# Kernel tuning notes

Measured on AMD Instinct MI355X. Metric: run time of the kernel, lower is better.

## Reference

```python
import jax, jax.numpy as jnp
import numpy as np

B, H, W, C, WS, NH, NL, ND = 64, 32, 32, 96, 8, 6, 4, 6
N = WS * WS
HD = C // NH
SC = HD ** -0.5


def _rel_pos_index():
    coords = np.stack(np.meshgrid(np.arange(WS), np.arange(WS), indexing='ij')).reshape(2, -1)
    rel = (coords[:, :, None] - coords[:, None, :]).transpose(1, 2, 0)
    rel[..., 0] += WS - 1
    rel[..., 1] += WS - 1
    rel[..., 0] *= 2 * WS - 1
    return jnp.asarray(rel.sum(-1))  # [N, N] int


def _attn_mask():
    shift = WS // 2
    img = np.zeros((H, W))
    cnt = 0
    for hs in (slice(0, -WS), slice(-WS, -shift), slice(-shift, None)):
        for ws_ in (slice(0, -WS), slice(-WS, -shift), slice(-shift, None)):
            img[hs, ws_] = cnt
            cnt += 1
    mw = img.reshape(H // WS, WS, W // WS, WS).transpose(0, 2, 1, 3).reshape(-1, N)
    am = mw[:, None, :] - mw[:, :, None]
    return jnp.asarray(np.where(am != 0, -100.0, 0.0).astype(np.float32))  # [nW, N, N]


RPI = _rel_pos_index()
AMASK = _attn_mask()


def ln(x, s, b):
    m = x.mean(-1, keepdims=True)
    v = ((x - m) ** 2).mean(-1, keepdims=True)
    return (x - m) * jax.lax.rsqrt(v + 1e-5) * s + b


def conv3(x, w, b):
    return jax.lax.conv_general_dilated(x, w, (1, 1), 'SAME', dimension_numbers=('NHWC', 'HWIO', 'NHWC')) + b


def win_part(x):  # (B,H,W,C) -> (B*nW, N, C)
    b = x.shape[0]
    return x.reshape(b, H // WS, WS, W // WS, WS, C).transpose(0, 1, 3, 2, 4, 5).reshape(-1, N, C)


def win_rev(xw, b):  # (B*nW, N, C) -> (B,H,W,C)
    return xw.reshape(b, H // WS, W // WS, WS, WS, C).transpose(0, 1, 3, 2, 4, 5).reshape(b, H, W, C)


def swin_block(x, shift, p):
    n1s, n1b, qw, qb, pw, pb, rpb, n2s, n2b, f1w, f1b, f2w, f2b = p
    b = x.shape[0]
    h = ln(x, n1s, n1b).reshape(b, H, W, C)
    if shift:
        h = jnp.roll(h, (-shift, -shift), (1, 2))
    xw = win_part(h)
    qkv = (xw @ qw + qb).reshape(-1, N, 3, NH, HD).transpose(2, 0, 3, 1, 4)
    q, k, v = qkv[0], qkv[1], qkv[2]  # each (B*nW, NH, N, HD)
    attn = (q * SC) @ k.transpose(0, 1, 3, 2)  # (B*nW, NH, N, N)
    bias = rpb[RPI.reshape(-1)].reshape(N, N, NH).transpose(2, 0, 1)
    attn = attn + bias[None]
    if shift:
        nW = AMASK.shape[0]
        attn = (attn.reshape(b, nW, NH, N, N) + AMASK[None, :, None]).reshape(-1, NH, N, N)
    attn = jax.nn.softmax(attn, -1)
    o = (attn @ v).transpose(0, 2, 1, 3).reshape(-1, N, C) @ pw + pb
    h = win_rev(o, b)
    if shift:
        h = jnp.roll(h, (shift, shift), (1, 2))
    x = x + h.reshape(b, H * W, C)
    y = ln(x, n2s, n2b)
    return x + jax.nn.gelu(y @ f1w + f1b, approximate=False) @ f2w + f2b


def setup_inputs() -> dict:
    key = jax.random.key(0)
    ks = iter(jax.random.split(key, 40))
    nrm = lambda shape: jax.random.normal(next(ks), shape, jnp.float32) * 0.02
    d = {
        'es_input': jax.random.normal(next(ks), (B, 2, H, W), jnp.float32),
        'j_plus_input': jax.random.normal(next(ks), (B, 2, H, W), jnp.float32),
        'conv_first_w': nrm((3, 3, 4, C)), 'conv_first_b': jnp.zeros((C,), jnp.float32),
        'pe_norm_s': jnp.ones((C,), jnp.float32), 'pe_norm_b': jnp.zeros((C,), jnp.float32),
        'n1_s': jnp.ones((NL, ND, C), jnp.float32), 'n1_b': jnp.zeros((NL, ND, C), jnp.float32),
        'qkv_w': nrm((NL, ND, C, 3 * C)), 'qkv_b': jnp.zeros((NL, ND, 3 * C), jnp.float32),
        'proj_w': nrm((NL, ND, C, C)), 'proj_b': jnp.zeros((NL, ND, C), jnp.float32),
        'rpb': nrm((NL, ND, (2 * WS - 1) ** 2, NH)),
        'n2_s': jnp.ones((NL, ND, C), jnp.float32), 'n2_b': jnp.zeros((NL, ND, C), jnp.float32),
        'fc1_w': nrm((NL, ND, C, 4 * C)), 'fc1_b': jnp.zeros((NL, ND, 4 * C), jnp.float32),
        'fc2_w': nrm((NL, ND, 4 * C, C)), 'fc2_b': jnp.zeros((NL, ND, C), jnp.float32),
        'rstb_conv_w': nrm((NL, 3, 3, C, C)), 'rstb_conv_b': jnp.zeros((NL, C), jnp.float32),
        'normf_s': jnp.ones((C,), jnp.float32), 'normf_b': jnp.zeros((C,), jnp.float32),
        'body_w': nrm((3, 3, C, C)), 'body_b': jnp.zeros((C,), jnp.float32),
        'last_w': nrm((3, 3, C, 2)), 'last_b': jnp.zeros((2,), jnp.float32),
    }
    return d


def reference(es_input, j_plus_input, conv_first_w, conv_first_b, pe_norm_s, pe_norm_b,
              n1_s, n1_b, qkv_w, qkv_b, proj_w, proj_b, rpb, n2_s, n2_b,
              fc1_w, fc1_b, fc2_w, fc2_b, rstb_conv_w, rstb_conv_b,
              normf_s, normf_b, body_w, body_b, last_w, last_b):
    x0 = jnp.concatenate([es_input, j_plus_input], 1).transpose(0, 2, 3, 1)  # NHWC, C=4
    xf = conv3(x0, conv_first_w, conv_first_b)  # shallow feature, [B,H,W,96]
    x = ln(xf.reshape(B, H * W, C), pe_norm_s, pe_norm_b)  # patch_embed norm
    for l in range(NL):
        r = x
        for d in range(ND):
            p = (n1_s[l, d], n1_b[l, d], qkv_w[l, d], qkv_b[l, d], proj_w[l, d], proj_b[l, d],
                 rpb[l, d], n2_s[l, d], n2_b[l, d], fc1_w[l, d], fc1_b[l, d], fc2_w[l, d], fc2_b[l, d])
            x = swin_block(x, 0 if d % 2 == 0 else WS // 2, p)
        x = conv3(x.reshape(B, H, W, C), rstb_conv_w[l], rstb_conv_b[l]).reshape(B, H * W, C) + r
    x = ln(x, normf_s, normf_b).reshape(B, H, W, C)
    res = conv3(x, body_w, body_b) + xf
    out = conv3(res, last_w, last_b)  # [B,H,W,2]
    return out.transpose(0, 3, 1, 2)
```

## Files before the change

kernel.cpp:

```cpp
#include <hip/hip_runtime.h>
#include <hip/hip_bf16.h>
#include <cstddef>
#include <cstdint>

#define BB 64
#define HH 32
#define WW_ 32
#define CC 96
#define WS 8
#define NH 6
#define NL 4
#define ND 6
#define T_TOK (BB*HH*WW_)
#define TC ((size_t)T_TOK*CC)

typedef long long ll;
typedef __attribute__((ext_vector_type(8))) short short8;
typedef __attribute__((ext_vector_type(4))) float f32x4;
typedef __attribute__((ext_vector_type(4))) unsigned short ushort4v;

__global__ void JNetSwinIR_41034117546277_kernel() {}

__device__ __forceinline__ unsigned short f2bf(float f) {
  unsigned u = __float_as_uint(f);
  unsigned r = (u + 0x7FFF + ((u >> 16) & 1)) >> 16;
  return (unsigned short)r;
}
__device__ __forceinline__ float bf2f(unsigned short h) {
  return __uint_as_float(((unsigned)h) << 16);
}

__global__ __launch_bounds__(256) void fill_kernel(float* p, float v, int n)
{
  const int idx = blockIdx.x * 256 + threadIdx.x;
  if (idx < n) p[idx] = v;
}

__global__ __launch_bounds__(256) void wconv_kernel(
    const float* __restrict__ W, unsigned short* __restrict__ Wt, int K, int N)
{
  const int ld = blockIdx.y;
  const int idx = blockIdx.x * 256 + threadIdx.x;
  if (idx >= K * N) return;
  const int k = idx / N, n = idx % N;
  Wt[(size_t)ld * K * N + (size_t)n * K + k] = f2bf(W[(size_t)ld * K * N + idx]);
}

__global__ __launch_bounds__(256) void wconv_conv_kernel(
    const float* __restrict__ W, unsigned short* __restrict__ Wt, int total)
{
  const int idx = blockIdx.x * 256 + threadIdx.x;
  if (idx >= total) return;
  const int l9 = idx / 9216;
  const int rest = idx % 9216;
  const int oc = rest / 96, ic = rest % 96;
  Wt[idx] = f2bf(W[(size_t)(l9 * 96 + ic) * 96 + oc]);
}

__global__ __launch_bounds__(256) void ln_fp32_kernel(
    const float* __restrict__ x, const float* __restrict__ gamma,
    const float* __restrict__ beta, float* __restrict__ out, float* out2)
{
  const int wave = threadIdx.x >> 6;
  const int lane = threadIdx.x & 63;
  const int t = blockIdx.x * 4 + wave;
  const float* xp = x + (size_t)t * CC;
  const float v0 = xp[lane];
  const float v1 = (lane < 32) ? xp[64 + lane] : 0.f;
  float s = v0 + v1, s2 = v0 * v0 + v1 * v1;
  #pragma unroll
  for (int off = 32; off; off >>= 1) {
    s  += __shfl_xor(s,  off);
    s2 += __shfl_xor(s2, off);
  }
  const float mean = s * (1.f / 96.f);
  const float var  = s2 * (1.f / 96.f) - mean * mean;
  const float inv  = rsqrtf(var + 1e-5f);
  const float r0 = (v0 - mean) * inv * gamma[lane] + beta[lane];
  const float r1 = (v1 - mean) * inv * gamma[64 + lane] + beta[64 + lane];
  out[(size_t)t * CC + lane] = r0;
  if (lane < 32) out[(size_t)t * CC + 64 + lane] = r1;
  if (out2) {
    out2[(size_t)t * CC + lane] = r0;
    if (lane < 32) out2[(size_t)t * CC + 64 + lane] = r1;
  }
}

__global__ __launch_bounds__(384) void swin_block_fused(
    float* x, const float* __restrict__ n1s, const float* __restrict__ n1b,
    const unsigned short* __restrict__ wq_ld, const float* __restrict__ qkvb,
    const float* __restrict__ rpb_ld,
    const unsigned short* __restrict__ wp_ld, const float* __restrict__ projb,
    const float* __restrict__ n2s, const float* __restrict__ n2b,
    const unsigned short* __restrict__ w1_ld, const float* __restrict__ f1b,
    const unsigned short* __restrict__ w2_ld, const float* __restrict__ f2b,
    int shift)
{
  const int widx = blockIdx.x;
  const int tid  = threadIdx.x;
  const int wv   = tid >> 6;
  const int lane = tid & 63;

  __shared__ __attribute__((aligned(16))) char smem[73496];
  auto a    = (unsigned short(*)[104])(smem);
  auto kk   = (unsigned short(*)[104])(smem + 13312);
  auto xacc = (float(*)[100])(smem + 13312);
  unsigned short* vvT = (unsigned short*)(smem + 26624);
  auto qt   = (unsigned short(*)[104])(smem + 40448);
  auto hbuf = (unsigned short(*)[200])(smem + 40448);
  unsigned short* pbuf = (unsigned short*)(smem + 53760);
  float* bias_s = (float*)(smem + 67584);
  int*   reg_s  = (int*)(smem + 72984);
  int*   st_s   = (int*)(smem + 73240);

  if (tid < 64) {
    const int wimg = widx & 15;
    const int h = (wimg >> 2) * 8 + (tid >> 3);
    const int w = (wimg & 3) * 8 + (tid & 7);
    reg_s[tid] = 3 * (h < 24 ? 0 : (h < 28 ? 1 : 2)) +
                     (w < 24 ? 0 : (w < 28 ? 1 : 2));
    const int b = widx >> 4;
    const int p = (h + shift) & 31, q = (w + shift) & 31;
    st_s[tid] = (b << 10) + (p << 5) + q;
  }
  for (int i = tid; i < NH * 225; i += 384) {
    const int hh = i / 225, ii = i % 225;
    bias_s[i] = rpb_ld[ii * NH + hh];
  }
  __syncthreads();

  for (int t = wv; t < 64; t += 6) {
    const float* xp = x + (size_t)st_s[t] * CC;
    const float v0 = xp[lane];
    const float v1 = (lane < 32) ? xp[64 + lane] : 0.f;
    float s = v0 + v1, s2 = v0 * v0 + v1 * v1;
    #pragma unroll
    for (int off = 32; off; off >>= 1) {
      s  += __shfl_xor(s,  off);
      s2 += __shfl_xor(s2, off);
    }
    const float mean = s * (1.f / 96.f);
    const float var  = s2 * (1.f / 96.f) - mean * mean;
    const float inv  = rsqrtf(var + 1e-5f);
    a[t][lane] = f2bf((v0 - mean) * inv * n1s[lane] + n1b[lane]);
    if (lane < 32)
      a[t][64 + lane] = f2bf((v1 - mean) * inv * n1s[64 + lane] + n1b[64 + lane]);
  }
  __syncthreads();

  {
    const int row = lane & 15;
    const int ko  = (lane >> 4) * 8;
    const int cc  = lane & 15;
    const int cr0 = (lane >> 4) * 4;
    #pragma unroll
    for (int out3 = 0; out3 < 3; ++out3) {
      const int n0 = out3 * 96 + wv * 16;
      const unsigned short* bp = wq_ld + (size_t)(n0 + row) * 96 + ko;
      const float bz = qkvb[n0 + cc];
      #pragma unroll
      for (int rt = 0; rt < 4; ++rt) {
        f32x4 acc = {0.f, 0.f, 0.f, 0.f};
        const unsigned short* ap = &a[rt * 16 + row][ko];
        #pragma unroll
        for (int k0 = 0; k0 < 96; k0 += 32) {
          const short8 af = *(const short8*)(ap + k0);
          const short8 bf = *(const short8*)(bp + k0);
          acc = __builtin_amdgcn_mfma_f32_16x16x32_bf16(af, bf, acc, 0, 0, 0);
        }
        #pragma unroll
        for (int r = 0; r < 4; ++r) {
          const int tok = rt * 16 + cr0 + r;
          const float v = acc[r] + bz;
          if (out3 == 0)      qt[tok][wv * 16 + cc] = f2bf(v);
          else if (out3 == 1) kk[tok][wv * 16 + cc] = f2bf(v);
          else                vvT[(wv * 16 + cc) * 72 + tok] = f2bf(v);
        }
      }
    }
  }
  __syncthreads();

  {
    const int head = wv;
    const int g  = lane >> 4;
    const int cc = lane & 15;
    const bool lo = (lane < 32);
    const float* bias_h = bias_s + head * 225;
    unsigned short* pb = pbuf + head * (16 * 72);
    const short8 z8 = {0, 0, 0, 0, 0, 0, 0, 0};
    short8 vf0, vf1;
    {
      const unsigned short* vp = vvT + (size_t)(head * 16 + cc) * 72 + g * 8;
      vf0 = *(const short8*)(vp);
      vf1 = *(const short8*)(vp + 32);
    }
    #pragma unroll
    for (int qtile = 0; qtile < 4; ++qtile) {
      short8 af = z8;
      if (lo) af = *(const short8*)&qt[qtile * 16 + cc][head * 16 + g * 8];
      f32x4 sa[4];
      #pragma unroll
      for (int kt = 0; kt < 4; ++kt) {
        short8 bf = z8;
        if (lo) bf = *(const short8*)&kk[kt * 16 + cc][head * 16 + g * 8];
        const f32x4 zero = {0.f, 0.f, 0.f, 0.f};
        sa[kt] = __builtin_amdgcn_mfma_f32_16x16x32_bf16(af, bf, zero, 0, 0, 0);
      }
      float p[4][4];
      #pragma unroll
      for (int r = 0; r < 4; ++r) {
        const int i = qtile * 16 + g * 4 + r;
        const int ih = i >> 3, iw = i & 7;
        const int ri = reg_s[i];
        float mx = -1e30f;
        #pragma unroll
        for (int kt = 0; kt < 4; ++kt) {
          const int j = kt * 16 + cc;
          const int idx = (ih - (j >> 3) + 7) * 15 + (iw - (j & 7) + 7);
          float v = sa[kt][r] * 0.25f + bias_h[idx];
          if (shift && reg_s[j] != ri) v -= 100.f;
          p[kt][r] = v;
          mx = fmaxf(mx, v);
        }
        mx = fmaxf(mx, __shfl_xor(mx, 1));
        mx = fmaxf(mx, __shfl_xor(mx, 2));
        mx = fmaxf(mx, __shfl_xor(mx, 4));
        mx = fmaxf(mx, __shfl_xor(mx, 8));
        float sum = 0.f;
        #pragma unroll
        for (int kt = 0; kt < 4; ++kt) {
          p[kt][r] = __expf(p[kt][r] - mx);
          sum += p[kt][r];
        }
        sum += __shfl_xor(sum, 1);
        sum += __shfl_xor(sum, 2);
        sum += __shfl_xor(sum, 4);
        sum += __shfl_xor(sum, 8);
        const float is = 1.f / sum;
        #pragma unroll
        for (int kt = 0; kt < 4; ++kt)
          pb[(g * 4 + r) * 72 + kt * 16 + cc] = f2bf(p[kt][r] * is);
      }
      f32x4 oa = {0.f, 0.f, 0.f, 0.f};
      {
        const unsigned short* pp = pb + cc * 72 + g * 8;
        const short8 pf0 = *(const short8*)(pp);
        const short8 pf1 = *(const short8*)(pp + 32);
        oa = __builtin_amdgcn_mfma_f32_16x16x32_bf16(pf0, vf0, oa, 0, 0, 0);
        oa = __builtin_amdgcn_mfma_f32_16x16x32_bf16(pf1, vf1, oa, 0, 0, 0);
      }
      #pragma unroll
      for (int r = 0; r < 4; ++r)
        a[qtile * 16 + g * 4 + r][head * 16 + cc] = f2bf(oa[r]);
    }
  }
  __syncthreads();

  {
    const int row = lane & 15;
    const int ko  = (lane >> 4) * 8;
    const int cc  = lane & 15;
    const int cr0 = (lane >> 4) * 4;
    const int n0 = wv * 16;
    const unsigned short* bp = wp_ld + (size_t)(n0 + row) * 96 + ko;
    const float bz = projb[n0 + cc];
    #pragma unroll
    for (int rt = 0; rt < 4; ++rt) {
      f32x4 acc = {0.f, 0.f, 0.f, 0.f};
      const unsigned short* ap = &a[rt * 16 + row][ko];
      #pragma unroll
      for (int k0 = 0; k0 < 96; k0 += 32) {
        const short8 af = *(const short8*)(ap + k0);
        const short8 bf = *(const short8*)(bp + k0);
        acc = __builtin_amdgcn_mfma_f32_16x16x32_bf16(af, bf, acc, 0, 0, 0);
      }
      #pragma unroll
      for (int r = 0; r < 4; ++r) {
        const int tok = rt * 16 + cr0 + r;
        const float xo = x[(size_t)st_s[tok] * CC + n0 + cc];
        xacc[tok][n0 + cc] = xo + acc[r] + bz;
      }
    }
  }
  __syncthreads();

  for (int t = wv; t < 64; t += 6) {
    const float v0 = xacc[t][lane];
    const float v1 = (lane < 32) ? xacc[t][64 + lane] : 0.f;
    float s = v0 + v1, s2 = v0 * v0 + v1 * v1;
    #pragma unroll
    for (int off = 32; off; off >>= 1) {
      s  += __shfl_xor(s,  off);
      s2 += __shfl_xor(s2, off);
    }
    const float mean = s * (1.f / 96.f);
    const float var  = s2 * (1.f / 96.f) - mean * mean;
    const float inv  = rsqrtf(var + 1e-5f);
    a[t][lane] = f2bf((v0 - mean) * inv * n2s[lane] + n2b[lane]);
    if (lane < 32)
      a[t][64 + lane] = f2bf((v1 - mean) * inv * n2s[64 + lane] + n2b[64 + lane]);
  }
  __syncthreads();

  const int row = lane & 15;
  const int ko  = (lane >> 4) * 8;
  const int cc  = lane & 15;
  const int cr0 = (lane >> 4) * 4;
  f32x4 acc2[4];
  #pragma unroll
  for (int i = 0; i < 4; ++i) acc2[i] = (f32x4){0.f, 0.f, 0.f, 0.f};
  #pragma unroll
  for (int p = 0; p < 2; ++p) {
    #pragma unroll
    for (int ct = 0; ct < 2; ++ct) {
      const int n0g = p * 192 + wv * 32 + ct * 16;
      const int n0l = wv * 32 + ct * 16;
      const unsigned short* bp = w1_ld + (size_t)(n0g + row) * 96 + ko;
      const float bz = f1b[n0g + cc];
      #pragma unroll
      for (int rt = 0; rt < 4; ++rt) {
        f32x4 acc = {0.f, 0.f, 0.f, 0.f};
        const unsigned short* ap = &a[rt * 16 + row][ko];
        #pragma unroll
        for (int k0 = 0; k0 < 96; k0 += 32) {
          const short8 af = *(const short8*)(ap + k0);
          const short8 bf = *(const short8*)(bp + k0);
          acc = __builtin_amdgcn_mfma_f32_16x16x32_bf16(af, bf, acc, 0, 0, 0);
        }
        #pragma unroll
        for (int r = 0; r < 4; ++r) {
          float v = acc[r] + bz;
          v = 0.5f * v * (1.f + erff(v * 0.70710678118f));
          hbuf[rt * 16 + cr0 + r][n0l + cc] = f2bf(v);
        }
      }
    }
    __syncthreads();
    {
      const int n0 = wv * 16;
      const unsigned short* bp = w2_ld + (size_t)(n0 + row) * 384 + p * 192 + ko;
      #pragma unroll
      for (int rt = 0; rt < 4; ++rt) {
        const unsigned short* ap = &hbuf[rt * 16 + row][ko];
        #pragma unroll
        for (int k0 = 0; k0 < 192; k0 += 32) {
          const short8 af = *(const short8*)(ap + k0);
          const short8 bf = *(const short8*)(bp + k0);
          acc2[rt] = __builtin_amdgcn_mfma_f32_16x16x32_bf16(af, bf, acc2[rt], 0, 0, 0);
        }
      }
    }
    __syncthreads();
  }

  {
    const int n0 = wv * 16;
    const float bz = f2b[n0 + cc];
    #pragma unroll
    for (int rt = 0; rt < 4; ++rt) {
      #pragma unroll
      for (int r = 0; r < 4; ++r) {
        const int tok = rt * 16 + cr0 + r;
        x[(size_t)st_s[tok] * CC + n0 + cc] = xacc[tok][n0 + cc] + acc2[rt][r] + bz;
      }
    }
  }
}

__global__ __launch_bounds__(256) void copy_kernel(
    float* __restrict__ dst, const float* __restrict__ src)
{
  const int idx = blockIdx.x * 256 + threadIdx.x;
  dst[idx] = src[idx];
}

__global__ __launch_bounds__(256) void conv96m_kernel(
    const float* __restrict__ x, const unsigned short* __restrict__ wt,
    const float* __restrict__ bias, const float* resid, float* out, float* out2)
{
  const int blk = blockIdx.x;
  const int b = blk >> 4, th = (blk >> 2) & 3, tw = blk & 3;
  const int h0 = th * 8, w0 = tw * 8;
  __shared__ unsigned short patch[100][104];
  for (int idx = threadIdx.x; idx < 100 * 24; idx += 256) {
    const int pp = idx / 24, c4 = (idx % 24) * 4;
    const int ph = pp / 10, pw = pp % 10;
    const int hh = h0 + ph - 1, ww = w0 + pw - 1;
    float4 v = {0.f, 0.f, 0.f, 0.f};
    if ((unsigned)hh < 32u && (unsigned)ww < 32u)
      v = *(const float4*)&x[(((size_t)b * 32 + hh) * 32 + ww) * 96 + c4];
    ushort4v o;
    o.x = f2bf(v.x); o.y = f2bf(v.y); o.z = f2bf(v.z); o.w = f2bf(v.w);
    *(ushort4v*)&patch[pp][c4] = o;
  }
  __syncthreads();
  const int wv = threadIdx.x >> 6, lane = threadIdx.x & 63;
  const int m0 = wv * 16;
  const int arow = lane & 15;
  const int ko  = (lane >> 4) * 8;
  const int px = m0 + arow;
  const int ph_ = px >> 3, pw_ = px & 7;
  f32x4 acc[6];
  #pragma unroll
  for (int i = 0; i < 6; ++i) acc[i] = (f32x4){0.f, 0.f, 0.f, 0.f};
  #pragma unroll
  for (int kh = 0; kh < 3; ++kh)
    #pragma unroll
    for (int kw = 0; kw < 3; ++kw) {
      const unsigned short* wbase = wt + (size_t)(kh * 3 + kw) * 9216;
      const unsigned short* prow = &patch[(ph_ + kh) * 10 + (pw_ + kw)][ko];
      #pragma unroll
      for (int k0 = 0; k0 < 96; k0 += 32) {
        const short8 af = *(const short8*)(prow + k0);
        #pragma unroll
        for (int nt = 0; nt < 6; ++nt) {
          const short8 bf = *(const short8*)(wbase + (size_t)(nt * 16 + arow) * 96 + ko + k0);
          acc[nt] = __builtin_amdgcn_mfma_f32_16x16x32_bf16(af, bf, acc[nt], 0, 0, 0);
        }
      }
    }
  const int cc = lane & 15;
  const int cr0 = (lane >> 4) * 4;
  #pragma unroll
  for (int nt = 0; nt < 6; ++nt) {
    const int oc = nt * 16 + cc;
    const float bz = bias[oc];
    #pragma unroll
    for (int r = 0; r < 4; ++r) {
      const int p = m0 + cr0 + r;
      const int h = p >> 3, w = p & 7;
      const size_t t = (((size_t)b * 32 + h0 + h) * 32 + (w0 + w));
      float v = acc[nt][r] + bz;
      if (resid) v += resid[t * 96 + oc];
      out[t * 96 + oc] = v;
      if (out2) out2[t * 96 + oc] = v;
    }
  }
}

__global__ __launch_bounds__(256) void conv_first_kernel(
    const float* __restrict__ es, const float* __restrict__ jp,
    const float* __restrict__ wgt, const float* __restrict__ bias,
    float* __restrict__ xf)
{
  const int idx = blockIdx.x * 256 + threadIdx.x;
  const int oc = idx % 96;
  const int pos = idx / 96;
  const int w = pos % 32, hp = (pos / 32) % 32, b = pos / 1024;
  float acc = bias[oc];
  for (int kh = 0; kh < 3; ++kh) {
    const int hh = hp + kh - 1;
    if ((unsigned)hh >= 32u) continue;
    for (int kw = 0; kw < 3; ++kw) {
      const int ww = w + kw - 1;
      if ((unsigned)ww >= 32u) continue;
      const size_t sp = ((size_t)b * 2 * 32 + hh) * 32 + ww;
      const float i0 = es[sp];
      const float i1 = es[sp + 1024];
      const float i2 = jp[sp];
      const float i3 = jp[sp + 1024];
      const float* wr = wgt + (size_t)((kh * 3 + kw) * 4) * 96 + oc;
      acc = fmaf(i0, wr[0], acc);
      acc = fmaf(i1, wr[96], acc);
      acc = fmaf(i2, wr[192], acc);
      acc = fmaf(i3, wr[288], acc);
    }
  }
  xf[idx] = acc;
}

__global__ __launch_bounds__(256) void conv_last_kernel(
    const float* __restrict__ res, const float* __restrict__ wgt,
    const float* __restrict__ bias, float* __restrict__ out)
{
  const int idx = blockIdx.x * 256 + threadIdx.x;
  const int oc = idx % 2;
  const int pos = idx / 2;
  const int w = pos % 32, hp = (pos / 32) % 32, b = pos / 1024;
  float acc = bias[oc];
  for (int kh = 0; kh < 3; ++kh) {
    const int hh = hp + kh - 1;
    if ((unsigned)hh >= 32u) continue;
    for (int kw = 0; kw < 3; ++kw) {
      const int ww = w + kw - 1;
      if ((unsigned)ww >= 32u) continue;
      const float* pr = res + (((size_t)b * 32 + hh) * 32 + ww) * 96;
      const float* wr = wgt + (size_t)((kh * 3 + kw) * 96) * 2 + oc;
      #pragma unroll 8
      for (int ic = 0; ic < 96; ++ic)
        acc = fmaf(pr[ic], wr[ic * 2], acc);
    }
  }
  out[(((size_t)b * 2 + oc) * 32 + hp) * 32 + w] = acc;
}

extern "C" void kernel_launch(void* const* d_in, const int* in_sizes, int n_in,
                              void* d_out, int out_size, void* d_ws, size_t ws_size,
                              hipStream_t stream)
{
  const int fill_grid = (out_size + 255) / 256;

  if (n_in != 27) {
    fill_kernel<<<fill_grid, 256, 0, stream>>>((float*)d_out, 200.0f + (float)n_in, out_size);
    return;
  }
  static const int expected_sizes[27] = {
    131072, 131072, 3456, 96, 96, 96, 2304, 2304, 663552, 6912,
    221184, 2304, 32400, 2304, 2304, 884736, 9216, 884736, 2304,
    331776, 384, 96, 96, 82944, 96, 1728, 2
  };
  for (int i = 0; i < 27; ++i) {
    if (in_sizes[i] != expected_sizes[i]) {
      fill_kernel<<<fill_grid, 256, 0, stream>>>((float*)d_out, 300.0f + (float)i, out_size);
      return;
    }
  }
  if (out_size != 131072) {
    fill_kernel<<<fill_grid, 256, 0, stream>>>((float*)d_out, 400.0f, out_size);
    return;
  }
  const uintptr_t raw = (uintptr_t)d_ws;
  const uintptr_t alignedp = (raw + 255) & ~(uintptr_t)255;
  const size_t ws_avail_bytes = (ws_size > (alignedp - raw)) ? ws_size - (alignedp - raw) : 0;
  const size_t avail = ws_avail_bytes / 4;
  const size_t WBUF_F = 1534464;
  if (avail < 2 * TC + WBUF_F) {
    fill_kernel<<<fill_grid, 256, 0, stream>>>((float*)d_out,
        100.0f + (float)(ws_size >> 20), out_size);
    return;
  }
  const bool rot = (avail >= 3 * TC + WBUF_F);

  const float* es      = (const float*)d_in[0];
  const float* jp      = (const float*)d_in[1];
  const float* cf_w    = (const float*)d_in[2];
  const float* cf_b    = (const float*)d_in[3];
  const float* pe_s    = (const float*)d_in[4];
  const float* pe_b    = (const float*)d_in[5];
  const float* n1_s    = (const float*)d_in[6];
  const float* n1_b    = (const float*)d_in[7];
  const float* qkv_w   = (const float*)d_in[8];
  const float* qkv_b   = (const float*)d_in[9];
  const float* proj_w  = (const float*)d_in[10];
  const float* proj_b  = (const float*)d_in[11];
  const float* rpb     = (const float*)d_in[12];
  const float* n2_s    = (const float*)d_in[13];
  const float* n2_b    = (const float*)d_in[14];
  const float* fc1_w   = (const float*)d_in[15];
  const float* fc1_b   = (const float*)d_in[16];
  const float* fc2_w   = (const float*)d_in[17];
  const float* fc2_b   = (const float*)d_in[18];
  const float* rstb_w  = (const float*)d_in[19];
  const float* rstb_b  = (const float*)d_in[20];
  const float* nf_s    = (const float*)d_in[21];
  const float* nf_b    = (const float*)d_in[22];
  const float* body_w  = (const float*)d_in[23];
  const float* body_b  = (const float*)d_in[24];
  const float* last_w  = (const float*)d_in[25];
  const float* last_b  = (const float*)d_in[26];

  float* base = (float*)alignedp;
  float* x  = base;
  float* r  = base + TC;
  float* sp = rot ? base + 2 * TC : nullptr;
  unsigned short* wq  = (unsigned short*)(base + (rot ? 3 : 2) * TC);
  unsigned short* wpj = wq + 663552;
  unsigned short* w1  = wpj + 221184;
  unsigned short* w2  = w1 + 884736;
  unsigned short* wcr = w2 + 884736;
  unsigned short* wcb = wcr + 331776;

  const int grid_tc = (int)(TC / 256);
  const int grid_lf = T_TOK / 4;
  const int nwin = T_TOK / 64;

  wconv_kernel<<<dim3((96 * 288 + 255) / 256, 24), 256, 0, stream>>>(qkv_w, wq, 96, 288);
  wconv_kernel<<<dim3((96 * 96 + 255) / 256, 24), 256, 0, stream>>>(proj_w, wpj, 96, 96);
  wconv_kernel<<<dim3((96 * 384 + 255) / 256, 24), 256, 0, stream>>>(fc1_w, w1, 96, 384);
  wconv_kernel<<<dim3((384 * 96 + 255) / 256, 24), 256, 0, stream>>>(fc2_w, w2, 384, 96);
  wconv_conv_kernel<<<(331776 + 255) / 256, 256, 0, stream>>>(rstb_w, wcr, 331776);
  wconv_conv_kernel<<<(82944 + 255) / 256, 256, 0, stream>>>(body_w, wcb, 82944);

  conv_first_kernel<<<grid_tc, 256, 0, stream>>>(es, jp, cf_w, cf_b, x);
  ln_fp32_kernel<<<grid_lf, 256, 0, stream>>>(x, pe_s, pe_b, x, rot ? r : nullptr);

  float* xb = x;
  float* rb = r;
  float* sb = sp;
  for (int l = 0; l < NL; ++l) {
    if (!rot) copy_kernel<<<grid_tc, 256, 0, stream>>>(rb, xb);
    for (int d = 0; d < ND; ++d) {
      const int ld = l * ND + d;
      const int shift = (d & 1) ? 4 : 0;
      swin_block_fused<<<nwin, 384, 0, stream>>>(
          xb, n1_s + ld * CC, n1_b + ld * CC,
          wq + (size_t)ld * 288 * 96, qkv_b + (size_t)ld * 288,
          rpb + (size_t)ld * 225 * NH,
          wpj + (size_t)ld * 96 * 96, proj_b + (size_t)ld * 96,
          n2_s + ld * CC, n2_b + ld * CC,
          w1 + (size_t)ld * 384 * 96, fc1_b + (size_t)ld * 384,
          w2 + (size_t)ld * 96 * 384, fc2_b + (size_t)ld * 96, shift);
    }
    if (rot) {
      conv96m_kernel<<<1024, 256, 0, stream>>>(xb, wcr + (size_t)l * 9 * 9216,
                                               rstb_b + (size_t)l * CC, rb, rb, sb);
      float* t = xb; xb = sb; sb = t;
    } else {
      conv96m_kernel<<<1024, 256, 0, stream>>>(xb, wcr + (size_t)l * 9 * 9216,
                                               rstb_b + (size_t)l * CC, rb, rb, nullptr);
      float* t = xb; xb = rb; rb = t;
    }
  }
  ln_fp32_kernel<<<grid_lf, 256, 0, stream>>>(xb, nf_s, nf_b, rb, nullptr);
  conv_first_kernel<<<grid_tc, 256, 0, stream>>>(es, jp, cf_w, cf_b, xb);
  conv96m_kernel<<<1024, 256, 0, stream>>>(rb, wcb, body_b, xb, xb, nullptr);
  conv_last_kernel<<<(BB * 32 * 32 * 2) / 256, 256, 0, stream>>>(xb, last_w, last_b, (float*)d_out);
}
```

Measured before the change: 3.890 ms.

## Shrink swin block LDS footprint and move to 8 waves per block

The fused Swin block kernel now runs 512 threads (8 waves) instead of 384. Its GEMM stages are re-tiled so that 16x16 output tiles are spread round-robin over the waves. The shared-memory footprint drops from about 73KB to about 54KB through several changes: the relative-position bias is pre-transposed by a new setup kernel and read from global memory, the attention probability buffer reuses the V region, and the MLP hidden buffer is chunked into four 96-wide passes. Together these aim to fit more blocks per CU and raise per-block parallelism. The cost is more barriers in the MLP loop, bias reads that now go to global or L2 memory, and some idle waves in the 6-head attention stage.

```diff
diff --git a/kernel.cpp b/kernel.cpp
--- a/kernel.cpp
+++ b/kernel.cpp
@@ -55,6 +55,16 @@
   const int rest = idx % 9216;
   const int oc = rest / 96, ic = rest % 96;
   Wt[idx] = f2bf(W[(size_t)(l9 * 96 + ic) * 96 + oc]);
+}
+
+__global__ __launch_bounds__(256) void rpbt_kernel(
+    const float* __restrict__ R, float* __restrict__ Rt)
+{
+  const int idx = blockIdx.x * 256 + threadIdx.x;
+  if (idx >= 24 * 1350) return;
+  const int ld = idx / 1350, rest = idx % 1350;
+  const int h = rest / 225, ii = rest % 225;
+  Rt[idx] = R[(size_t)ld * 1350 + ii * 6 + h];
 }
 
 __global__ __launch_bounds__(256) void ln_fp32_kernel(
@@ -86,10 +96,10 @@
   }
 }
 
-__global__ __launch_bounds__(384) void swin_block_fused(
+__global__ __launch_bounds__(512) void swin_block_fused(
     float* x, const float* __restrict__ n1s, const float* __restrict__ n1b,
     const unsigned short* __restrict__ wq_ld, const float* __restrict__ qkvb,
-    const float* __restrict__ rpb_ld,
+    const float* __restrict__ rpbt_ld,
     const unsigned short* __restrict__ wp_ld, const float* __restrict__ projb,
     const float* __restrict__ n2s, const float* __restrict__ n2b,
     const unsigned short* __restrict__ w1_ld, const float* __restrict__ f1b,
@@ -101,35 +111,34 @@
   const int wv   = tid >> 6;
   const int lane = tid & 63;
 
-  __shared__ __attribute__((aligned(16))) char smem[73496];
+  __shared__ __attribute__((aligned(16))) char smem[54016];
   auto a    = (unsigned short(*)[104])(smem);
   auto kk   = (unsigned short(*)[104])(smem + 13312);
   auto xacc = (float(*)[100])(smem + 13312);
   unsigned short* vvT = (unsigned short*)(smem + 26624);
   auto qt   = (unsigned short(*)[104])(smem + 40448);
-  auto hbuf = (unsigned short(*)[200])(smem + 40448);
-  unsigned short* pbuf = (unsigned short*)(smem + 53760);
-  float* bias_s = (float*)(smem + 67584);
-  int*   reg_s  = (int*)(smem + 72984);
-  int*   st_s   = (int*)(smem + 73240);
+  auto hbuf = (unsigned short(*)[104])(smem + 40448);
+  unsigned short* st_s = (unsigned short*)(smem + 53760);
+  short*          reg_s = (short*)(smem + 53888);
 
   if (tid < 64) {
     const int wimg = widx & 15;
     const int h = (wimg >> 2) * 8 + (tid >> 3);
     const int w = (wimg & 3) * 8 + (tid & 7);
-    reg_s[tid] = 3 * (h < 24 ? 0 : (h < 28 ? 1 : 2)) +
-                     (w < 24 ? 0 : (w < 28 ? 1 : 2));
+    reg_s[tid] = (short)(3 * (h < 24 ? 0 : (h < 28 ? 1 : 2)) +
+                             (w < 24 ? 0 : (w < 28 ? 1 : 2)));
     const int b = widx >> 4;
     const int p = (h + shift) & 31, q = (w + shift) & 31;
-    st_s[tid] = (b << 10) + (p << 5) + q;
-  }
-  for (int i = tid; i < NH * 225; i += 384) {
-    const int hh = i / 225, ii = i % 225;
-    bias_s[i] = rpb_ld[ii * NH + hh];
+    st_s[tid] = (unsigned short)((b << 10) + (p << 5) + q);
   }
   __syncthreads();
 
-  for (int t = wv; t < 64; t += 6) {
+  const int row = lane & 15;
+  const int ko  = (lane >> 4) * 8;
+  const int cc  = lane & 15;
+  const int cr0 = (lane >> 4) * 4;
+
+  for (int t = wv; t < 64; t += 8) {
     const float* xp = x + (size_t)st_s[t] * CC;
     const float v0 = xp[lane];
     const float v1 = (lane < 32) ? xp[64 + lane] : 0.f;
@@ -148,46 +157,36 @@
   }
   __syncthreads();
 
-  {
-    const int row = lane & 15;
-    const int ko  = (lane >> 4) * 8;
-    const int cc  = lane & 15;
-    const int cr0 = (lane >> 4) * 4;
-    #pragma unroll
-    for (int out3 = 0; out3 < 3; ++out3) {
-      const int n0 = out3 * 96 + wv * 16;
-      const unsigned short* bp = wq_ld + (size_t)(n0 + row) * 96 + ko;
-      const float bz = qkvb[n0 + cc];
-      #pragma unroll
-      for (int rt = 0; rt < 4; ++rt) {
-        f32x4 acc = {0.f, 0.f, 0.f, 0.f};
-        const unsigned short* ap = &a[rt * 16 + row][ko];
-        #pragma unroll
-        for (int k0 = 0; k0 < 96; k0 += 32) {
-          const short8 af = *(const short8*)(ap + k0);
-          const short8 bf = *(const short8*)(bp + k0);
-          acc = __builtin_amdgcn_mfma_f32_16x16x32_bf16(af, bf, acc, 0, 0, 0);
-        }
-        #pragma unroll
-        for (int r = 0; r < 4; ++r) {
-          const int tok = rt * 16 + cr0 + r;
-          const float v = acc[r] + bz;
-          if (out3 == 0)      qt[tok][wv * 16 + cc] = f2bf(v);
-          else if (out3 == 1) kk[tok][wv * 16 + cc] = f2bf(v);
-          else                vvT[(wv * 16 + cc) * 72 + tok] = f2bf(v);
-        }
-      }
+  for (int tt = wv; tt < 72; tt += 8) {
+    const int rt = tt / 18, ct = tt % 18;
+    const int n0g = ct * 16;
+    const unsigned short* bp = wq_ld + (size_t)(n0g + row) * 96 + ko;
+    const float bz = qkvb[n0g + cc];
+    f32x4 acc = {0.f, 0.f, 0.f, 0.f};
+    const unsigned short* ap = &a[rt * 16 + row][ko];
+    #pragma unroll
+    for (int k0 = 0; k0 < 96; k0 += 32) {
+      const short8 af = *(const short8*)(ap + k0);
+      const short8 bf = *(const short8*)(bp + k0);
+      acc = __builtin_amdgcn_mfma_f32_16x16x32_bf16(af, bf, acc, 0, 0, 0);
+    }
+    #pragma unroll
+    for (int r = 0; r < 4; ++r) {
+      const int tok = rt * 16 + cr0 + r;
+      const float v = acc[r] + bz;
+      if (ct < 6)       qt[tok][ct * 16 + cc] = f2bf(v);
+      else if (ct < 12) kk[tok][(ct - 6) * 16 + cc] = f2bf(v);
+      else              vvT[((ct - 12) * 16 + cc) * 72 + tok] = f2bf(v);
     }
   }
   __syncthreads();
 
-  {
+  if (wv < 6) {
     const int head = wv;
     const int g  = lane >> 4;
-    const int cc = lane & 15;
     const bool lo = (lane < 32);
-    const float* bias_h = bias_s + head * 225;
-    unsigned short* pb = pbuf + head * (16 * 72);
+    const float* bias_h = rpbt_ld + head * 225;
+    unsigned short* pb = vvT + head * (16 * 72);
     const short8 z8 = {0, 0, 0, 0, 0, 0, 0, 0};
     short8 vf0, vf1;
     {
@@ -257,16 +256,55 @@
   }
   __syncthreads();
 
-  {
-    const int row = lane & 15;
-    const int ko  = (lane >> 4) * 8;
-    const int cc  = lane & 15;
-    const int cr0 = (lane >> 4) * 4;
-    const int n0 = wv * 16;
+  for (int tt = wv; tt < 24; tt += 8) {
+    const int rt = tt / 6, ct = tt % 6;
+    const int n0 = ct * 16;
     const unsigned short* bp = wp_ld + (size_t)(n0 + row) * 96 + ko;
     const float bz = projb[n0 + cc];
-    #pragma unroll
-    for (int rt = 0; rt < 4; ++rt) {
+    f32x4 acc = {0.f, 0.f, 0.f, 0.f};
+    const unsigned short* ap = &a[rt * 16 + row][ko];
+    #pragma unroll
+    for (int k0 = 0; k0 < 96; k0 += 32) {
+      const short8 af = *(const short8*)(ap + k0);
+      const short8 bf = *(const short8*)(bp + k0);
+      acc = __builtin_amdgcn_mfma_f32_16x16x32_bf16(af, bf, acc, 0, 0, 0);
+    }
+    #pragma unroll
+    for (int r = 0; r < 4; ++r) {
+      const int tok = rt * 16 + cr0 + r;
+      const float xo = x[(size_t)st_s[tok] * CC + n0 + cc];
+      xacc[tok][n0 + cc] = xo + acc[r] + bz;
+    }
+  }
+  __syncthreads();
+
+  for (int t = wv; t < 64; t += 8) {
+    const float v0 = xacc[t][lane];
+    const float v1 = (lane < 32) ? xacc[t][64 + lane] : 0.f;
+    float s = v0 + v1, s2 = v0 * v0 + v1 * v1;
+    #pragma unroll
+    for (int off = 32; off; off >>= 1) {
+      s  += __shfl_xor(s,  off);
+      s2 += __shfl_xor(s2, off);
+    }
+    const float mean = s * (1.f / 96.f);
+    const float var  = s2 * (1.f / 96.f) - mean * mean;
+    const float inv  = rsqrtf(var + 1e-5f);
+    a[t][lane] = f2bf((v0 - mean) * inv * n2s[lane] + n2b[lane]);
+    if (lane < 32)
+      a[t][64 + lane] = f2bf((v1 - mean) * inv * n2s[64 + lane] + n2b[64 + lane]);
+  }
+  __syncthreads();
+
+  f32x4 acc2[3];
+  #pragma unroll
+  for (int i = 0; i < 3; ++i) acc2[i] = (f32x4){0.f, 0.f, 0.f, 0.f};
+  for (int p = 0; p < 4; ++p) {
+    for (int tt = wv; tt < 24; tt += 8) {
+      const int rt = tt / 6, ct = tt % 6;
+      const int n0g = p * 96 + ct * 16;
+      const unsigned short* bp = w1_ld + (size_t)(n0g + row) * 96 + ko;
+      const float bz = f1b[n0g + cc];
       f32x4 acc = {0.f, 0.f, 0.f, 0.f};
       const unsigned short* ap = &a[rt * 16 + row][ko];
       #pragma unroll
@@ -277,93 +315,38 @@
       }
       #pragma unroll
       for (int r = 0; r < 4; ++r) {
-        const int tok = rt * 16 + cr0 + r;
-        const float xo = x[(size_t)st_s[tok] * CC + n0 + cc];
-        xacc[tok][n0 + cc] = xo + acc[r] + bz;
+        float v = acc[r] + bz;
+        v = 0.5f * v * (1.f + erff(v * 0.70710678118f));
+        hbuf[rt * 16 + cr0 + r][ct * 16 + cc] = f2bf(v);
       }
     }
-  }
-  __syncthreads();
-
-  for (int t = wv; t < 64; t += 6) {
-    const float v0 = xacc[t][lane];
-    const float v1 = (lane < 32) ? xacc[t][64 + lane] : 0.f;
-    float s = v0 + v1, s2 = v0 * v0 + v1 * v1;
-    #pragma unroll
-    for (int off = 32; off; off >>= 1) {
-      s  += __shfl_xor(s,  off);
-      s2 += __shfl_xor(s2, off);
-    }
-    const float mean = s * (1.f / 96.f);
-    const float var  = s2 * (1.f / 96.f) - mean * mean;
-    const float inv  = rsqrtf(var + 1e-5f);
-    a[t][lane] = f2bf((v0 - mean) * inv * n2s[lane] + n2b[lane]);
-    if (lane < 32)
-      a[t][64 + lane] = f2bf((v1 - mean) * inv * n2s[64 + lane] + n2b[64 + lane]);
-  }
-  __syncthreads();
-
-  const int row = lane & 15;
-  const int ko  = (lane >> 4) * 8;
-  const int cc  = lane & 15;
-  const int cr0 = (lane >> 4) * 4;
-  f32x4 acc2[4];
+    __syncthreads();
+    #pragma unroll
+    for (int i = 0; i < 3; ++i) {
+      const int tt2 = wv * 3 + i;
+      const int rt = tt2 / 6, ct = tt2 % 6;
+      const unsigned short* bp = w2_ld + (size_t)(ct * 16 + row) * 384 + p * 96 + ko;
+      const unsigned short* ap = &hbuf[rt * 16 + row][ko];
+      #pragma unroll
+      for (int k0 = 0; k0 < 96; k0 += 32) {
+        const short8 af = *(const short8*)(ap + k0);
+        const short8 bf = *(const short8*)(bp + k0);
+        acc2[i] = __builtin_amdgcn_mfma_f32_16x16x32_bf16(af, bf, acc2[i], 0, 0, 0);
+      }
+    }
+    __syncthreads();
+  }
+
   #pragma unroll
-  for (int i = 0; i < 4; ++i) acc2[i] = (f32x4){0.f, 0.f, 0.f, 0.f};
-  #pragma unroll
-  for (int p = 0; p < 2; ++p) {
-    #pragma unroll
-    for (int ct = 0; ct < 2; ++ct) {
-      const int n0g = p * 192 + wv * 32 + ct * 16;
-      const int n0l = wv * 32 + ct * 16;
-      const unsigned short* bp = w1_ld + (size_t)(n0g + row) * 96 + ko;
-      const float bz = f1b[n0g + cc];
-      #pragma unroll
-      for (int rt = 0; rt < 4; ++rt) {
-        f32x4 acc = {0.f, 0.f, 0.f, 0.f};
-        const unsigned short* ap = &a[rt * 16 + row][ko];
-        #pragma unroll
-        for (int k0 = 0; k0 < 96; k0 += 32) {
-          const short8 af = *(const short8*)(ap + k0);
-          const short8 bf = *(const short8*)(bp + k0);
-          acc = __builtin_amdgcn_mfma_f32_16x16x32_bf16(af, bf, acc, 0, 0, 0);
-        }
-        #pragma unroll
-        for (int r = 0; r < 4; ++r) {
-          float v = acc[r] + bz;
-          v = 0.5f * v * (1.f + erff(v * 0.70710678118f));
-          hbuf[rt * 16 + cr0 + r][n0l + cc] = f2bf(v);
-        }
-      }
-    }
-    __syncthreads();
-    {
-      const int n0 = wv * 16;
-      const unsigned short* bp = w2_ld + (size_t)(n0 + row) * 384 + p * 192 + ko;
-      #pragma unroll
-      for (int rt = 0; rt < 4; ++rt) {
-        const unsigned short* ap = &hbuf[rt * 16 + row][ko];
-        #pragma unroll
-        for (int k0 = 0; k0 < 192; k0 += 32) {
-          const short8 af = *(const short8*)(ap + k0);
-          const short8 bf = *(const short8*)(bp + k0);
-          acc2[rt] = __builtin_amdgcn_mfma_f32_16x16x32_bf16(af, bf, acc2[rt], 0, 0, 0);
-        }
-      }
-    }
-    __syncthreads();
-  }
-
-  {
-    const int n0 = wv * 16;
+  for (int i = 0; i < 3; ++i) {
+    const int tt2 = wv * 3 + i;
+    const int rt = tt2 / 6, ct = tt2 % 6;
+    const int n0 = ct * 16;
     const float bz = f2b[n0 + cc];
     #pragma unroll
-    for (int rt = 0; rt < 4; ++rt) {
-      #pragma unroll
-      for (int r = 0; r < 4; ++r) {
-        const int tok = rt * 16 + cr0 + r;
-        x[(size_t)st_s[tok] * CC + n0 + cc] = xacc[tok][n0 + cc] + acc2[rt][r] + bz;
-      }
+    for (int r = 0; r < 4; ++r) {
+      const int tok = rt * 16 + cr0 + r;
+      x[(size_t)st_s[tok] * CC + n0 + cc] = xacc[tok][n0 + cc] + acc2[i][r] + bz;
     }
   }
 }
@@ -524,7 +507,7 @@
   const uintptr_t alignedp = (raw + 255) & ~(uintptr_t)255;
   const size_t ws_avail_bytes = (ws_size > (alignedp - raw)) ? ws_size - (alignedp - raw) : 0;
   const size_t avail = ws_avail_bytes / 4;
-  const size_t WBUF_F = 1534464;
+  const size_t WBUF_F = 1534464 + 32400;
   if (avail < 2 * TC + WBUF_F) {
     fill_kernel<<<fill_grid, 256, 0, stream>>>((float*)d_out,
         100.0f + (float)(ws_size >> 20), out_size);
@@ -570,6 +553,7 @@
   unsigned short* w2  = w1 + 884736;
   unsigned short* wcr = w2 + 884736;
   unsigned short* wcb = wcr + 331776;
+  float* rpbt = (float*)(wcb + 82944);
 
   const int grid_tc = (int)(TC / 256);
   const int grid_lf = T_TOK / 4;
@@ -581,6 +565,7 @@
   wconv_kernel<<<dim3((384 * 96 + 255) / 256, 24), 256, 0, stream>>>(fc2_w, w2, 384, 96);
   wconv_conv_kernel<<<(331776 + 255) / 256, 256, 0, stream>>>(rstb_w, wcr, 331776);
   wconv_conv_kernel<<<(82944 + 255) / 256, 256, 0, stream>>>(body_w, wcb, 82944);
+  rpbt_kernel<<<(24 * 1350 + 255) / 256, 256, 0, stream>>>(rpb, rpbt);
 
   conv_first_kernel<<<grid_tc, 256, 0, stream>>>(es, jp, cf_w, cf_b, x);
   ln_fp32_kernel<<<grid_lf, 256, 0, stream>>>(x, pe_s, pe_b, x, rot ? r : nullptr);
@@ -593,10 +578,10 @@
     for (int d = 0; d < ND; ++d) {
       const int ld = l * ND + d;
       const int shift = (d & 1) ? 4 : 0;
-      swin_block_fused<<<nwin, 384, 0, stream>>>(
+      swin_block_fused<<<nwin, 512, 0, stream>>>(
           xb, n1_s + ld * CC, n1_b + ld * CC,
           wq + (size_t)ld * 288 * 96, qkv_b + (size_t)ld * 288,
-          rpb + (size_t)ld * 225 * NH,
+          rpbt + (size_t)ld * 1350,
           wpj + (size_t)ld * 96 * 96, proj_b + (size_t)ld * 96,
           n2_s + ld * CC, n2_b + ld * CC,
           w1 + (size_t)ld * 384 * 96, fc1_b + (size_t)ld * 384,
```

New measurement: 3.327 ms, median of 3. 1.17x faster.
